# Kernel optimization log

Hardware: AMD Instinct MI355X
Metric: run time of the kernel (lower is better)

## Reference

```python
import jax, jax.numpy as jnp
import numpy as np

N, HID, L, NC = 2048, 256, 4, 10
D0, D1, D2 = HID, HID // 2, HID // 8   # dims for degrees l=0,1,2
H, DH = 4, HID // 4                    # heads for degree-0 attention
F = D0 + D1 + D2                       # invariant feature width
C2 = float(np.sqrt(3.0))


def setup_inputs() -> dict:
    key = jax.random.key(0)
    ks = jax.random.split(key, 16)

    def w(k, shape, fan):
        return jax.random.normal(k, shape, jnp.float32) / np.float32(np.sqrt(fan))

    return {
        "x": jax.random.uniform(ks[0], (N, 118), jnp.float32),
        "pos": jax.random.normal(ks[1], (N, 3), jnp.float32) * 3.0,
        "emb_W": w(ks[2], (118, D0), 118),
        "emb_b": jnp.zeros((D0,), jnp.float32),
        "Wq": w(ks[3], (L, F, H * DH), F),
        "Wk": w(ks[4], (L, F, H * DH), F),
        "Wv0": w(ks[5], (L, D0, D0), D0),
        "Wv1": w(ks[6], (L, D1, D1), D1),
        "Wv2": w(ks[7], (L, D2, D2), D2),
        "Ws1": w(ks[8], (L, D0, D1), D0),
        "Ws2": w(ks[9], (L, D0, D2), D0),
        "Wffa": w(ks[10], (L, D0, 2 * D0), D0),
        "Wffb": w(ks[11], (L, 2 * D0, D0), 2 * D0),
        "Wg": w(ks[12], (L, F, D1 + D2), F),
        "out_W": w(ks[13], (D0, NC), D0),
        "out_b": jnp.zeros((NC,), jnp.float32),
    }


def _sph_harmonics(pos):
    """Real spherical harmonics Y1 [N,N,3], Y2 [N,N,5] of pairwise unit vectors."""
    rel = pos[None, :, :] - pos[:, None, :]                  # [N,N,3]
    dist = jnp.linalg.norm(rel, axis=-1, keepdims=True)
    valid = (dist > 1e-6).astype(pos.dtype)                  # zero out self-pairs
    u = rel / jnp.maximum(dist, 1e-6) * valid
    ux, uy, uz = u[..., 0], u[..., 1], u[..., 2]
    Y1 = u
    Y2 = jnp.stack([
        C2 * ux * uy,
        C2 * uy * uz,
        0.5 * (3.0 * uz * uz - 1.0),
        C2 * ux * uz,
        0.5 * C2 * (ux * ux - uy * uy),
    ], axis=-1) * valid                                      # [N,N,5]
    return Y1, Y2


def _invariants(x0, x1, x2):
    return jnp.concatenate([
        x0,
        jnp.linalg.norm(x1, axis=-1),
        jnp.linalg.norm(x2, axis=-1),
    ], axis=-1)                                              # [N,F]


def _layer(x0, x1, x2, Y1, Y2, Wq, Wk, Wv0, Wv1, Wv2, Ws1, Ws2, Wffa, Wffb, Wg):
    inv = _invariants(x0, x1, x2)
    q = (inv @ Wq).reshape(N, H, DH)
    k = (inv @ Wk).reshape(N, H, DH)
    attn = jax.nn.softmax(jnp.einsum('nhd,mhd->hnm', q, k) / np.float32(np.sqrt(DH)), axis=-1)

    # degree-0 aggregation (4 heads)
    v0 = (x0 @ Wv0).reshape(N, H, D0 // H)
    agg0 = jnp.einsum('hnm,mhc->nhc', attn, v0).reshape(N, D0)

    a = attn.mean(0)                                         # [N,N] single head for l>0
    # degree-1: channel-mixed values + degree-0 -> degree-1 via Y1
    v1 = jnp.einsum('mdc,de->mec', x1, Wv1)                  # [N,D1,3]
    agg1 = jnp.einsum('nm,mdc->ndc', a, v1)
    mix1 = jnp.einsum('nmc,md->ndc', a[:, :, None] * Y1, x0 @ Ws1)
    # degree-2: channel-mixed values + degree-0 -> degree-2 via Y2
    v2 = jnp.einsum('mdc,de->mec', x2, Wv2)                  # [N,D2,5]
    agg2 = jnp.einsum('nm,mdc->ndc', a, v2)
    mix2 = jnp.einsum('nmc,md->ndc', a[:, :, None] * Y2, x0 @ Ws2)

    x0 = x0 + agg0
    x1 = x1 + agg1 + mix1
    x2 = x2 + agg2 + mix2

    # gated equivariant feedforward
    x0 = x0 + jax.nn.silu(x0 @ Wffa) @ Wffb
    g = jax.nn.sigmoid(_invariants(x0, x1, x2) @ Wg)         # [N,D1+D2]
    x1 = x1 * g[:, :D1, None]
    x2 = x2 * g[:, D1:, None]
    return x0, x1, x2


def reference(x, pos, emb_W, emb_b, Wq, Wk, Wv0, Wv1, Wv2, Ws1, Ws2, Wffa, Wffb, Wg, out_W, out_b):
    Y1, Y2 = _sph_harmonics(pos)
    x0 = x @ emb_W + emb_b                                   # input embedding
    x1 = jnp.zeros((N, D1, 3), x0.dtype)
    x2 = jnp.zeros((N, D2, 5), x0.dtype)
    for l in range(L):
        x0, x1, x2 = _layer(x0, x1, x2, Y1, Y2,
                            Wq[l], Wk[l], Wv0[l], Wv1[l], Wv2[l],
                            Ws1[l], Ws2[l], Wffa[l], Wffb[l], Wg[l])
    return x0 @ out_W + out_b                                # [N, num_classes]
```

## Files before the change

### kernel.cpp

```cpp
#include <hip/hip_runtime.h>
#include <math.h>

#define N_    2048
#define D0_   256
#define D1_   128
#define D2_   32
#define F_    416
#define H_    4
#define DH_   64
#define L_    4
#define NC_   10
#define C2_   1.7320508075688772f
#define X12W  544

typedef unsigned short u16;
typedef __attribute__((ext_vector_type(8))) short short8v;
typedef __attribute__((ext_vector_type(4))) float f32x4;

union U8 { u16 u[8]; short8v v; };

__device__ __forceinline__ u16 f2bf(float f) {
    union { float f; unsigned int u; } x; x.f = f;
    unsigned int r = x.u + 0x7FFFu + ((x.u >> 16) & 1u);
    return (u16)(r >> 16);
}
__device__ __forceinline__ float bf2f(u16 u) {
    union { float f; unsigned int u; } x; x.u = ((unsigned int)u) << 16;
    return x.f;
}

__device__ __forceinline__ f32x4 mfma16(short8v a, short8v b, f32x4 c) {
    return __builtin_amdgcn_mfma_f32_16x16x32_bf16(a, b, c, 0, 0, 0);
}

enum { B_NN = 0, B_NT = 1 };
enum { EPI_STORE = 0, EPI_SILU = 1, EPI_SIGMOID = 2, EPI_ACCUM = 3, EPI_ATOMIC = 4,
       EPI_STOREB = 5 };

template<int BLAY, int EPI>
__global__ __launch_bounds__(256) void mfma_gemm(
    const float* __restrict__ A, int lda,
    const float* __restrict__ B, int ldb,
    const float* __restrict__ bias,
    float* __restrict__ C, int ldc,
    int M, int K, int Nn, float scale, int kchunk)
{
    __shared__ __align__(16) u16 As[64][40];
    __shared__ __align__(16) u16 Bs[64][40];
    const int t = threadIdx.x;
    const int bm = blockIdx.y * 64, bn = blockIdx.x * 64;
    const int lane = t & 63, w = t >> 6;
    const int r0 = (w >> 1) * 32, c0 = (w & 1) * 32;
    const int fr = lane & 15, fk = (lane >> 4) * 8;
    const int ml = t >> 2, k8 = (t & 3) * 8;
    const int kbeg = blockIdx.z * kchunk;
    const int kend = (kbeg + kchunk < K) ? kbeg + kchunk : K;
    f32x4 acc[2][2] = {};

    for (int k0 = kbeg; k0 < kend; k0 += 32) {
        {
            U8 u;
            if (((lda & 3) == 0) && (k0 + 32 <= kend)) {
                const float* ap = A + (size_t)(bm + ml) * lda + k0 + k8;
                float4 a0 = *(const float4*)ap;
                float4 a1 = *(const float4*)(ap + 4);
                u.u[0]=f2bf(a0.x); u.u[1]=f2bf(a0.y); u.u[2]=f2bf(a0.z); u.u[3]=f2bf(a0.w);
                u.u[4]=f2bf(a1.x); u.u[5]=f2bf(a1.y); u.u[6]=f2bf(a1.z); u.u[7]=f2bf(a1.w);
            } else {
#pragma unroll
                for (int j = 0; j < 8; ++j) {
                    int kk = k0 + k8 + j;
                    u.u[j] = f2bf(kk < kend ? A[(size_t)(bm + ml) * lda + kk] : 0.f);
                }
            }
            *(short8v*)&As[ml][k8] = u.v;
        }
        {
            U8 u;
            if (BLAY == B_NT) {
                if (((ldb & 3) == 0) && (k0 + 32 <= kend) && (bn + ml < Nn)) {
                    const float* bp = B + (size_t)(bn + ml) * ldb + k0 + k8;
                    float4 b0 = *(const float4*)bp;
                    float4 b1 = *(const float4*)(bp + 4);
                    u.u[0]=f2bf(b0.x); u.u[1]=f2bf(b0.y); u.u[2]=f2bf(b0.z); u.u[3]=f2bf(b0.w);
                    u.u[4]=f2bf(b1.x); u.u[5]=f2bf(b1.y); u.u[6]=f2bf(b1.z); u.u[7]=f2bf(b1.w);
                } else {
#pragma unroll
                    for (int j = 0; j < 8; ++j) {
                        int kk = k0 + k8 + j;
                        u.u[j] = f2bf((kk < kend && bn + ml < Nn)
                                      ? B[(size_t)(bn + ml) * ldb + kk] : 0.f);
                    }
                }
            } else {
                int nc = bn + ml;
#pragma unroll
                for (int j = 0; j < 8; ++j) {
                    int kk = k0 + k8 + j;
                    u.u[j] = f2bf((kk < kend && nc < Nn) ? B[(size_t)kk * ldb + nc] : 0.f);
                }
            }
            *(short8v*)&Bs[ml][k8] = u.v;
        }
        __syncthreads();
        short8v a0 = *(const short8v*)&As[r0 + fr][fk];
        short8v a1 = *(const short8v*)&As[r0 + 16 + fr][fk];
        short8v b0 = *(const short8v*)&Bs[c0 + fr][fk];
        short8v b1 = *(const short8v*)&Bs[c0 + 16 + fr][fk];
        acc[0][0] = mfma16(a0, b0, acc[0][0]);
        acc[0][1] = mfma16(a0, b1, acc[0][1]);
        acc[1][0] = mfma16(a1, b0, acc[1][0]);
        acc[1][1] = mfma16(a1, b1, acc[1][1]);
        __syncthreads();
    }
#pragma unroll
    for (int mi = 0; mi < 2; ++mi)
#pragma unroll
    for (int ni = 0; ni < 2; ++ni)
#pragma unroll
    for (int r = 0; r < 4; ++r) {
        int row = bm + r0 + mi * 16 + ((lane >> 4) << 2) + r;
        int col = bn + c0 + ni * 16 + fr;
        if (col >= Nn) continue;
        float v = acc[mi][ni][r];
        if (EPI == EPI_STOREB) {
            ((u16*)C)[(size_t)row * ldc + col] = f2bf(v * scale);
        } else {
            float* cp = C + (size_t)row * ldc + col;
            if (EPI == EPI_STORE)   *cp = v * scale + (bias ? bias[col] : 0.f);
            if (EPI == EPI_SILU)    *cp = v / (1.f + expf(-v));
            if (EPI == EPI_SIGMOID) *cp = 1.f / (1.f + expf(-v));
            if (EPI == EPI_ACCUM)   *cp += v;
            if (EPI == EPI_ATOMIC)  atomicAdd(cp, v);
        }
    }
}

template<int NB, int EPI>
__global__ __launch_bounds__(256) void aggP(
    const u16* __restrict__ A, int lda,
    const float* __restrict__ B, int ldb,
    float* __restrict__ C, int ldc,
    int K, int Nn, int kchunk)
{
    __shared__ __align__(16) u16 As[64][40];
    __shared__ __align__(16) u16 Bs[NB][64][40];
    const int t = threadIdx.x;
    const int bm = blockIdx.y * 64, bn0 = blockIdx.x * 64 * NB;
    const int lane = t & 63, w = t >> 6;
    const int r0 = (w >> 1) * 32, c0 = (w & 1) * 32;
    const int fr = lane & 15, fk = (lane >> 4) * 8;
    const int ml = t >> 2, k8 = (t & 3) * 8;
    const int kbeg = blockIdx.z * kchunk;
    const int kend = (kbeg + kchunk < K) ? kbeg + kchunk : K;
    f32x4 acc[NB][2][2] = {};

    for (int k0 = kbeg; k0 < kend; k0 += 32) {
        *(short8v*)&As[ml][k8] = *(const short8v*)(A + (size_t)(bm + ml) * lda + k0 + k8);
#pragma unroll
        for (int nb = 0; nb < NB; ++nb) {
            int nc = bn0 + nb * 64 + ml;
            U8 u;
#pragma unroll
            for (int j = 0; j < 8; ++j) {
                int kk = k0 + k8 + j;
                u.u[j] = f2bf(nc < Nn ? B[(size_t)kk * ldb + nc] : 0.f);
            }
            *(short8v*)&Bs[nb][ml][k8] = u.v;
        }
        __syncthreads();
        short8v a0 = *(const short8v*)&As[r0 + fr][fk];
        short8v a1 = *(const short8v*)&As[r0 + 16 + fr][fk];
#pragma unroll
        for (int nb = 0; nb < NB; ++nb) {
            short8v b0 = *(const short8v*)&Bs[nb][c0 + fr][fk];
            short8v b1 = *(const short8v*)&Bs[nb][c0 + 16 + fr][fk];
            acc[nb][0][0] = mfma16(a0, b0, acc[nb][0][0]);
            acc[nb][0][1] = mfma16(a0, b1, acc[nb][0][1]);
            acc[nb][1][0] = mfma16(a1, b0, acc[nb][1][0]);
            acc[nb][1][1] = mfma16(a1, b1, acc[nb][1][1]);
        }
        __syncthreads();
    }
#pragma unroll
    for (int nb = 0; nb < NB; ++nb)
#pragma unroll
    for (int mi = 0; mi < 2; ++mi)
#pragma unroll
    for (int ni = 0; ni < 2; ++ni)
#pragma unroll
    for (int r = 0; r < 4; ++r) {
        int row = bm + r0 + mi * 16 + ((lane >> 4) << 2) + r;
        int col = bn0 + nb * 64 + c0 + ni * 16 + fr;
        if (col >= Nn) continue;
        float v = acc[nb][mi][ni][r];
        float* cp = C + (size_t)row * ldc + col;
        if (EPI == EPI_ATOMIC) atomicAdd(cp, v);
        else                   *cp += v;
    }
}

__global__ void ucompute_kernel(const float* __restrict__ pos, u16* __restrict__ U) {
    int idx = blockIdx.x * 256 + threadIdx.x;
    int n = idx >> 11, m = idx & (N_ - 1);
    float rx = pos[m * 3 + 0] - pos[n * 3 + 0];
    float ry = pos[m * 3 + 1] - pos[n * 3 + 1];
    float rz = pos[m * 3 + 2] - pos[n * 3 + 2];
    float d2 = rx * rx + ry * ry + rz * rz;
    bool valid = d2 > 1e-12f;
    float rinv = valid ? rsqrtf(d2) : 0.f;
    size_t base = (size_t)n * N_ + m;
    const size_t CS = (size_t)N_ * N_;
    U[base]          = f2bf(rx * rinv);
    U[base + CS]     = f2bf(ry * rinv);
    U[base + 2 * CS] = f2bf(rz * rinv);
}

__global__ __launch_bounds__(256) void mix1_kernel(
    const u16* __restrict__ amb, const u16* __restrict__ U,
    const float* __restrict__ s1, float* __restrict__ x12)
{
    const int gx = blockIdx.x;
    const int colbase = (gx & 1) * 64, ks = gx >> 1;
    const int bm = blockIdx.y * 64;
    const size_t CS = (size_t)N_ * N_;
    __shared__ __align__(16) u16 As[3][64][40];
    __shared__ __align__(16) u16 Bs[64][40];
    const int t = threadIdx.x, lane = t & 63, w = t >> 6;
    const int r0 = (w >> 1) * 32, c0 = (w & 1) * 32;
    const int fr = lane & 15, fk = (lane >> 4) * 8;
    const int ml = t >> 2, k8 = (t & 3) * 8;
    const int kbeg = ks * 512, kend = kbeg + 512;
    f32x4 acc[3][2][2] = {};

    for (int m0 = kbeg; m0 < kend; m0 += 32) {
        const size_t off = (size_t)(bm + ml) * N_ + m0 + k8;
        U8 am8; am8.v = *(const short8v*)(amb + off);
        U8 xv, yv, zv;
        xv.v = *(const short8v*)(U + off);
        yv.v = *(const short8v*)(U + CS + off);
        zv.v = *(const short8v*)(U + 2 * CS + off);
        U8 o0, o1, o2;
#pragma unroll
        for (int j = 0; j < 8; ++j) {
            float a = bf2f(am8.u[j]);
            o0.u[j] = f2bf(a * bf2f(xv.u[j]));
            o1.u[j] = f2bf(a * bf2f(yv.u[j]));
            o2.u[j] = f2bf(a * bf2f(zv.u[j]));
        }
        *(short8v*)&As[0][ml][k8] = o0.v;
        *(short8v*)&As[1][ml][k8] = o1.v;
        *(short8v*)&As[2][ml][k8] = o2.v;
        {
            int nc = colbase + ml;
            U8 u;
#pragma unroll
            for (int j = 0; j < 8; ++j)
                u.u[j] = f2bf(s1[(size_t)(m0 + k8 + j) * 128 + nc]);
            *(short8v*)&Bs[ml][k8] = u.v;
        }
        __syncthreads();
        short8v b0 = *(const short8v*)&Bs[c0 + fr][fk];
        short8v b1 = *(const short8v*)&Bs[c0 + 16 + fr][fk];
#pragma unroll
        for (int c = 0; c < 3; ++c) {
            short8v a0 = *(const short8v*)&As[c][r0 + fr][fk];
            short8v a1 = *(const short8v*)&As[c][r0 + 16 + fr][fk];
            acc[c][0][0] = mfma16(a0, b0, acc[c][0][0]);
            acc[c][0][1] = mfma16(a0, b1, acc[c][0][1]);
            acc[c][1][0] = mfma16(a1, b0, acc[c][1][0]);
            acc[c][1][1] = mfma16(a1, b1, acc[c][1][1]);
        }
        __syncthreads();
    }
#pragma unroll
    for (int c = 0; c < 3; ++c)
#pragma unroll
    for (int mi = 0; mi < 2; ++mi)
#pragma unroll
    for (int ni = 0; ni < 2; ++ni)
#pragma unroll
    for (int r = 0; r < 4; ++r) {
        int row = bm + r0 + mi * 16 + ((lane >> 4) << 2) + r;
        int col = colbase + c0 + ni * 16 + fr;
        atomicAdd(&x12[(size_t)row * X12W + col * 3 + c], acc[c][mi][ni][r]);
    }
}

__global__ __launch_bounds__(256) void mix2_kernel(
    const u16* __restrict__ amb, const u16* __restrict__ U,
    const float* __restrict__ s2, float* __restrict__ x12)
{
    const int ks = blockIdx.x;
    const int bm = blockIdx.y * 64;
    const size_t CS = (size_t)N_ * N_;
    __shared__ __align__(16) u16 As[5][64][40];
    __shared__ __align__(16) u16 Bs[64][40];
    const int t = threadIdx.x, lane = t & 63, w = t >> 6;
    const int r0 = (w >> 1) * 32, c0 = (w & 1) * 32;
    const int fr = lane & 15, fk = (lane >> 4) * 8;
    const int ml = t >> 2, k8 = (t & 3) * 8;
    const int kbeg = ks * 256, kend = kbeg + 256;
    f32x4 acc[5][2][2] = {};

    for (int m0 = kbeg; m0 < kend; m0 += 32) {
        const size_t off = (size_t)(bm + ml) * N_ + m0 + k8;
        U8 am8; am8.v = *(const short8v*)(amb + off);
        U8 xv, yv, zv;
        xv.v = *(const short8v*)(U + off);
        yv.v = *(const short8v*)(U + CS + off);
        zv.v = *(const short8v*)(U + 2 * CS + off);
        U8 o[5];
#pragma unroll
        for (int j = 0; j < 8; ++j) {
            float a = bf2f(am8.u[j]);
            float ux = bf2f(xv.u[j]), uy = bf2f(yv.u[j]), uz = bf2f(zv.u[j]);
            o[0].u[j] = f2bf(a * C2_ * ux * uy);
            o[1].u[j] = f2bf(a * C2_ * uy * uz);
            o[2].u[j] = f2bf((ux*ux + uy*uy + uz*uz > 0.5f)
                             ? a * 0.5f * (3.f * uz * uz - 1.f) : 0.f);
            o[3].u[j] = f2bf(a * C2_ * ux * uz);
            o[4].u[j] = f2bf(a * 0.5f * C2_ * (ux * ux - uy * uy));
        }
#pragma unroll
        for (int c = 0; c < 5; ++c) *(short8v*)&As[c][ml][k8] = o[c].v;
        {
            int nc = ml;
            U8 u;
#pragma unroll
            for (int j = 0; j < 8; ++j)
                u.u[j] = f2bf(nc < 32 ? s2[(size_t)(m0 + k8 + j) * 32 + nc] : 0.f);
            *(short8v*)&Bs[ml][k8] = u.v;
        }
        __syncthreads();
        short8v b0 = *(const short8v*)&Bs[c0 + fr][fk];
        short8v b1 = *(const short8v*)&Bs[c0 + 16 + fr][fk];
#pragma unroll
        for (int c = 0; c < 5; ++c) {
            short8v a0 = *(const short8v*)&As[c][r0 + fr][fk];
            short8v a1 = *(const short8v*)&As[c][r0 + 16 + fr][fk];
            acc[c][0][0] = mfma16(a0, b0, acc[c][0][0]);
            acc[c][0][1] = mfma16(a0, b1, acc[c][0][1]);
            acc[c][1][0] = mfma16(a1, b0, acc[c][1][0]);
            acc[c][1][1] = mfma16(a1, b1, acc[c][1][1]);
        }
        __syncthreads();
    }
#pragma unroll
    for (int c = 0; c < 5; ++c)
#pragma unroll
    for (int mi = 0; mi < 2; ++mi)
#pragma unroll
    for (int ni = 0; ni < 2; ++ni)
#pragma unroll
    for (int r = 0; r < 4; ++r) {
        int row = bm + r0 + mi * 16 + ((lane >> 4) << 2) + r;
        int col = c0 + ni * 16 + fr;
        if (col < 32)
            atomicAdd(&x12[(size_t)row * X12W + 384 + col * 5 + c], acc[c][mi][ni][r]);
    }
}

__global__ void invar_kernel(const float* __restrict__ x0, const float* __restrict__ x12,
                             float* __restrict__ inv) {
    int n = blockIdx.x, t = threadIdx.x;
    inv[(size_t)n * F_ + t] = x0[(size_t)n * D0_ + t];
    if (t < 128) {
        const float* p = x12 + (size_t)n * X12W + t * 3;
        inv[(size_t)n * F_ + 256 + t] = sqrtf(p[0]*p[0] + p[1]*p[1] + p[2]*p[2]);
    }
    if (t < 32) {
        const float* p = x12 + (size_t)n * X12W + 384 + t * 5;
        inv[(size_t)n * F_ + 384 + t] =
            sqrtf(p[0]*p[0] + p[1]*p[1] + p[2]*p[2] + p[3]*p[3] + p[4]*p[4]);
    }
}

__global__ void v1_kernel(const float* __restrict__ x12, const float* __restrict__ W,
                          float* __restrict__ Vflat) {
    int m = blockIdx.x, t = threadIdx.x;
    __shared__ float sh[384];
    sh[t] = x12[(size_t)m * X12W + t];
    __syncthreads();
    int e = t / 3, c = t % 3;
    float acc = 0.f;
#pragma unroll 4
    for (int d = 0; d < 128; ++d)
        acc = fmaf(sh[d * 3 + c], W[d * 128 + e], acc);
    Vflat[(size_t)m * X12W + t] = acc;
}

__global__ void v2_kernel(const float* __restrict__ x12, const float* __restrict__ W,
                          float* __restrict__ Vflat) {
    int m = blockIdx.x, t = threadIdx.x;
    __shared__ float sh[160];
    if (t < 160) sh[t] = x12[(size_t)m * X12W + 384 + t];
    __syncthreads();
    if (t < 160) {
        int e = t / 5, c = t % 5;
        float acc = 0.f;
#pragma unroll 4
        for (int d = 0; d < 32; ++d)
            acc = fmaf(sh[d * 5 + c], W[d * 32 + e], acc);
        Vflat[(size_t)m * X12W + 384 + t] = acc;
    }
}

__global__ void softmax4(u16* __restrict__ Sb, u16* __restrict__ amb) {
    int n = blockIdx.x, t = threadIdx.x;
    __shared__ float red[256];
    const size_t NN = (size_t)N_ * N_;
    float amv[8] = {};
    for (int h = 0; h < H_; ++h) {
        u16* Sp = Sb + (size_t)h * NN + (size_t)n * N_ + t * 8;
        U8 sv; sv.v = *(const short8v*)Sp;
        float s[8];
#pragma unroll
        for (int j = 0; j < 8; ++j) s[j] = bf2f(sv.u[j]);
        float mx = s[0];
#pragma unroll
        for (int j = 1; j < 8; ++j) mx = fmaxf(mx, s[j]);
        red[t] = mx; __syncthreads();
        for (int st = 128; st > 0; st >>= 1) { if (t < st) red[t] = fmaxf(red[t], red[t + st]); __syncthreads(); }
        mx = red[0]; __syncthreads();
        float sum = 0.f;
#pragma unroll
        for (int j = 0; j < 8; ++j) { s[j] = expf(s[j] - mx); sum += s[j]; }
        red[t] = sum; __syncthreads();
        for (int st = 128; st > 0; st >>= 1) { if (t < st) red[t] += red[t + st]; __syncthreads(); }
        float rinv = 1.f / red[0]; __syncthreads();
        U8 pv;
#pragma unroll
        for (int j = 0; j < 8; ++j) {
            float p = s[j] * rinv;
            pv.u[j] = f2bf(p);
            amv[j] += 0.25f * p;
        }
        *(short8v*)Sp = pv.v;
    }
    U8 av;
#pragma unroll
    for (int j = 0; j < 8; ++j) av.u[j] = f2bf(amv[j]);
    *(short8v*)(amb + (size_t)n * N_ + t * 8) = av.v;
}

__global__ void gate_kernel(const float* __restrict__ g, float* __restrict__ x12) {
    int idx = blockIdx.x * 256 + threadIdx.x;
    if (idx >= N_ * X12W) return;
    int n = idx / X12W, j = idx % X12W;
    float gv = (j < 384) ? g[n * 160 + j / 3] : g[n * 160 + 128 + (j - 384) / 5];
    x12[idx] *= gv;
}

extern "C" void kernel_launch(void* const* d_in, const int* in_sizes, int n_in,
                              void* d_out, int out_size, void* d_ws, size_t ws_size,
                              hipStream_t stream) {
    const float* x    = (const float*)d_in[0];
    const float* pos  = (const float*)d_in[1];
    const float* embW = (const float*)d_in[2];
    const float* embB = (const float*)d_in[3];
    const float* Wq   = (const float*)d_in[4];
    const float* Wk   = (const float*)d_in[5];
    const float* Wv0  = (const float*)d_in[6];
    const float* Wv1  = (const float*)d_in[7];
    const float* Wv2  = (const float*)d_in[8];
    const float* Ws1  = (const float*)d_in[9];
    const float* Ws2  = (const float*)d_in[10];
    const float* Wffa = (const float*)d_in[11];
    const float* Wffb = (const float*)d_in[12];
    const float* Wg   = (const float*)d_in[13];
    const float* outW = (const float*)d_in[14];
    const float* outB = (const float*)d_in[15];
    float* out = (float*)d_out;

    const size_t NN = (size_t)N_ * N_;
    float* p = (float*)d_ws;
    float* x0    = p; p += N_ * D0_;
    float* x12   = p; p += N_ * X12W;
    float* inv   = p; p += N_ * F_;
    float* q     = p; p += N_ * D0_;
    float* k     = p; p += N_ * D0_;
    float* v0    = p; p += N_ * D0_;
    float* Vflat = p; p += N_ * X12W;
    float* s1    = p; p += N_ * D1_;
    float* s2    = p; p += N_ * D2_;
    float* fft   = p; p += N_ * 512;
    float* gm    = p; p += N_ * 160;
    u16* ub  = (u16*)p;
    u16* Sb  = ub; ub += 4 * NN;
    u16* amb = ub; ub += NN;
    u16* U   = ub;

    hipMemsetAsync(x12, 0, (size_t)N_ * X12W * sizeof(float), stream);
    ucompute_kernel<<<(N_ * N_) / 256, 256, 0, stream>>>(pos, U);

    mfma_gemm<B_NN, EPI_STORE><<<dim3(4, 32), 256, 0, stream>>>(
        x, 118, embW, 256, embB, x0, 256, N_, 118, 256, 1.f, 118);

    for (int l = 0; l < L_; ++l) {
        const float* Wq_l   = Wq   + (size_t)l * F_ * 256;
        const float* Wk_l   = Wk   + (size_t)l * F_ * 256;
        const float* Wv0_l  = Wv0  + (size_t)l * 256 * 256;
        const float* Wv1_l  = Wv1  + (size_t)l * 128 * 128;
        const float* Wv2_l  = Wv2  + (size_t)l * 32 * 32;
        const float* Ws1_l  = Ws1  + (size_t)l * 256 * 128;
        const float* Ws2_l  = Ws2  + (size_t)l * 256 * 32;
        const float* Wffa_l = Wffa + (size_t)l * 256 * 512;
        const float* Wffb_l = Wffb + (size_t)l * 512 * 256;
        const float* Wg_l   = Wg   + (size_t)l * F_ * 160;

        invar_kernel<<<N_, 256, 0, stream>>>(x0, x12, inv);
        mfma_gemm<B_NN, EPI_STORE><<<dim3(4, 32), 256, 0, stream>>>(
            inv, F_, Wq_l, 256, nullptr, q, 256, N_, F_, 256, 1.f, F_);
        mfma_gemm<B_NN, EPI_STORE><<<dim3(4, 32), 256, 0, stream>>>(
            inv, F_, Wk_l, 256, nullptr, k, 256, N_, F_, 256, 1.f, F_);
        mfma_gemm<B_NN, EPI_STORE><<<dim3(4, 32), 256, 0, stream>>>(
            x0, 256, Wv0_l, 256, nullptr, v0, 256, N_, 256, 256, 1.f, 256);
        mfma_gemm<B_NN, EPI_STORE><<<dim3(2, 32), 256, 0, stream>>>(
            x0, 256, Ws1_l, 128, nullptr, s1, 128, N_, 256, 128, 1.f, 256);
        mfma_gemm<B_NN, EPI_STORE><<<dim3(1, 32), 256, 0, stream>>>(
            x0, 256, Ws2_l, 32, nullptr, s2, 32, N_, 256, 32, 1.f, 256);
        v1_kernel<<<N_, 384, 0, stream>>>(x12, Wv1_l, Vflat);
        v2_kernel<<<N_, 192, 0, stream>>>(x12, Wv2_l, Vflat);

        for (int h = 0; h < H_; ++h)
            mfma_gemm<B_NT, EPI_STOREB><<<dim3(32, 32), 256, 0, stream>>>(
                q + h * 64, 256, k + h * 64, 256, nullptr,
                (float*)(Sb + (size_t)h * NN), N_, N_, 64, N_, 0.125f, 64);
        softmax4<<<N_, 256, 0, stream>>>(Sb, amb);
        for (int h = 0; h < H_; ++h)
            aggP<1, EPI_ATOMIC><<<dim3(1, 32, 8), 256, 0, stream>>>(
                Sb + (size_t)h * NN, N_, v0 + h * 64, 256, x0 + h * 64, 256,
                N_, 64, 256);

        aggP<3, EPI_ATOMIC><<<dim3(3, 32, 3), 256, 0, stream>>>(
            amb, N_, Vflat, X12W, x12, X12W, N_, X12W, 704);
        mix1_kernel<<<dim3(8, 32), 256, 0, stream>>>(amb, U, s1, x12);
        mix2_kernel<<<dim3(8, 32), 256, 0, stream>>>(amb, U, s2, x12);

        mfma_gemm<B_NN, EPI_SILU><<<dim3(8, 32), 256, 0, stream>>>(
            x0, 256, Wffa_l, 512, nullptr, fft, 512, N_, 256, 512, 1.f, 256);
        mfma_gemm<B_NN, EPI_ACCUM><<<dim3(4, 32), 256, 0, stream>>>(
            fft, 512, Wffb_l, 256, nullptr, x0, 256, N_, 512, 256, 1.f, 512);

        invar_kernel<<<N_, 256, 0, stream>>>(x0, x12, inv);
        mfma_gemm<B_NN, EPI_SIGMOID><<<dim3(3, 32), 256, 0, stream>>>(
            inv, F_, Wg_l, 160, nullptr, gm, 160, N_, F_, 160, 1.f, F_);
        gate_kernel<<<(N_ * X12W + 255) / 256, 256, 0, stream>>>(gm, x12);
    }

    mfma_gemm<B_NN, EPI_STORE><<<dim3(1, 32), 256, 0, stream>>>(
        x0, 256, outW, NC_, outB, out, NC_, N_, 256, NC_, 1.f, 256);
}
```

Before: 1.766 ms.

## Batch per-head launches via grid z and merge mix kernels into channel-parallel grid

Adds head/k-split decoding of blockIdx.z to the GEMM and aggregation kernels so the four per-head score GEMMs and four aggregation launches become single launches. It merges mix1 and mix2 into one kernel that assigns one spherical-harmonic channel per z-slice, which raises block count but makes each block re-read amb and s1/s2. It also changes the aggP<3> k-split from 3 to 4 chunks. The aim is fewer launches and better occupancy on the GPU, at the cost of redundant global loads per channel.

```diff
diff --git a/kernel.cpp b/kernel.cpp
--- a/kernel.cpp
+++ b/kernel.cpp
@@ -43,17 +43,20 @@
     const float* __restrict__ B, int ldb,
     const float* __restrict__ bias,
     float* __restrict__ C, int ldc,
-    int M, int K, int Nn, float scale, int kchunk)
+    int M, int K, int Nn, float scale, int kchunk,
+    int zk, long long Ah, long long Bh, long long Ch)
 {
     __shared__ __align__(16) u16 As[64][40];
     __shared__ __align__(16) u16 Bs[64][40];
     const int t = threadIdx.x;
     const int bm = blockIdx.y * 64, bn = blockIdx.x * 64;
+    const int hz = blockIdx.z / zk, kz = blockIdx.z % zk;
+    A += (size_t)hz * Ah; B += (size_t)hz * Bh;
     const int lane = t & 63, w = t >> 6;
     const int r0 = (w >> 1) * 32, c0 = (w & 1) * 32;
     const int fr = lane & 15, fk = (lane >> 4) * 8;
     const int ml = t >> 2, k8 = (t & 3) * 8;
-    const int kbeg = blockIdx.z * kchunk;
+    const int kbeg = kz * kchunk;
     const int kend = (kbeg + kchunk < K) ? kbeg + kchunk : K;
     f32x4 acc[2][2] = {};
 
@@ -124,9 +127,9 @@
         if (col >= Nn) continue;
         float v = acc[mi][ni][r];
         if (EPI == EPI_STOREB) {
-            ((u16*)C)[(size_t)row * ldc + col] = f2bf(v * scale);
+            ((u16*)C + (size_t)hz * Ch)[(size_t)row * ldc + col] = f2bf(v * scale);
         } else {
-            float* cp = C + (size_t)row * ldc + col;
+            float* cp = C + (size_t)hz * Ch + (size_t)row * ldc + col;
             if (EPI == EPI_STORE)   *cp = v * scale + (bias ? bias[col] : 0.f);
             if (EPI == EPI_SILU)    *cp = v / (1.f + expf(-v));
             if (EPI == EPI_SIGMOID) *cp = 1.f / (1.f + expf(-v));
@@ -141,17 +144,20 @@
     const u16* __restrict__ A, int lda,
     const float* __restrict__ B, int ldb,
     float* __restrict__ C, int ldc,
-    int K, int Nn, int kchunk)
+    int K, int Nn, int kchunk,
+    int zk, long long Ah, long long Bh, long long Ch)
 {
     __shared__ __align__(16) u16 As[64][40];
     __shared__ __align__(16) u16 Bs[NB][64][40];
     const int t = threadIdx.x;
     const int bm = blockIdx.y * 64, bn0 = blockIdx.x * 64 * NB;
+    const int hz = blockIdx.z / zk, kz = blockIdx.z % zk;
+    A += (size_t)hz * Ah; B += (size_t)hz * Bh; C += (size_t)hz * Ch;
     const int lane = t & 63, w = t >> 6;
     const int r0 = (w >> 1) * 32, c0 = (w & 1) * 32;
     const int fr = lane & 15, fk = (lane >> 4) * 8;
     const int ml = t >> 2, k8 = (t & 3) * 8;
-    const int kbeg = blockIdx.z * kchunk;
+    const int kbeg = kz * kchunk;
     const int kend = (kbeg + kchunk < K) ? kbeg + kchunk : K;
     f32x4 acc[NB][2][2] = {};
 
@@ -216,65 +222,79 @@
     U[base + 2 * CS] = f2bf(rz * rinv);
 }
 
-__global__ __launch_bounds__(256) void mix1_kernel(
+__global__ __launch_bounds__(256) void mixc_kernel(
     const u16* __restrict__ amb, const u16* __restrict__ U,
-    const float* __restrict__ s1, float* __restrict__ x12)
+    const float* __restrict__ s1, const float* __restrict__ s2,
+    float* __restrict__ x12)
 {
+    const int ch = blockIdx.z;
     const int gx = blockIdx.x;
-    const int colbase = (gx & 1) * 64, ks = gx >> 1;
     const int bm = blockIdx.y * 64;
     const size_t CS = (size_t)N_ * N_;
-    __shared__ __align__(16) u16 As[3][64][40];
+    const bool deg1 = ch < 3;
+    const int colbase = deg1 ? (gx & 1) * 64 : 0;
+    const int ks      = deg1 ? (gx >> 1) : gx;
+    const int kchunk  = deg1 ? 512 : 256;
+    const float* Bp   = deg1 ? s1 : s2;
+    const int Bld     = deg1 ? 128 : 32;
+    __shared__ __align__(16) u16 As[64][40];
     __shared__ __align__(16) u16 Bs[64][40];
     const int t = threadIdx.x, lane = t & 63, w = t >> 6;
     const int r0 = (w >> 1) * 32, c0 = (w & 1) * 32;
     const int fr = lane & 15, fk = (lane >> 4) * 8;
     const int ml = t >> 2, k8 = (t & 3) * 8;
-    const int kbeg = ks * 512, kend = kbeg + 512;
-    f32x4 acc[3][2][2] = {};
+    const int kbeg = ks * kchunk, kend = kbeg + kchunk;
+    f32x4 acc[2][2] = {};
 
     for (int m0 = kbeg; m0 < kend; m0 += 32) {
         const size_t off = (size_t)(bm + ml) * N_ + m0 + k8;
         U8 am8; am8.v = *(const short8v*)(amb + off);
-        U8 xv, yv, zv;
-        xv.v = *(const short8v*)(U + off);
-        yv.v = *(const short8v*)(U + CS + off);
-        zv.v = *(const short8v*)(U + 2 * CS + off);
-        U8 o0, o1, o2;
-#pragma unroll
-        for (int j = 0; j < 8; ++j) {
-            float a = bf2f(am8.u[j]);
-            o0.u[j] = f2bf(a * bf2f(xv.u[j]));
-            o1.u[j] = f2bf(a * bf2f(yv.u[j]));
-            o2.u[j] = f2bf(a * bf2f(zv.u[j]));
-        }
-        *(short8v*)&As[0][ml][k8] = o0.v;
-        *(short8v*)&As[1][ml][k8] = o1.v;
-        *(short8v*)&As[2][ml][k8] = o2.v;
+        U8 o;
+        if (deg1) {
+            U8 uv; uv.v = *(const short8v*)(U + (size_t)ch * CS + off);
+#pragma unroll
+            for (int j = 0; j < 8; ++j)
+                o.u[j] = f2bf(bf2f(am8.u[j]) * bf2f(uv.u[j]));
+        } else {
+            U8 xv, yv, zv;
+            xv.v = *(const short8v*)(U + off);
+            yv.v = *(const short8v*)(U + CS + off);
+            zv.v = *(const short8v*)(U + 2 * CS + off);
+#pragma unroll
+            for (int j = 0; j < 8; ++j) {
+                float a = bf2f(am8.u[j]);
+                float ux = bf2f(xv.u[j]), uy = bf2f(yv.u[j]), uz = bf2f(zv.u[j]);
+                float y;
+                if      (ch == 3) y = C2_ * ux * uy;
+                else if (ch == 4) y = C2_ * uy * uz;
+                else if (ch == 5) y = (ux*ux + uy*uy + uz*uz > 0.5f)
+                                      ? 0.5f * (3.f * uz * uz - 1.f) : 0.f;
+                else if (ch == 6) y = C2_ * ux * uz;
+                else              y = 0.5f * C2_ * (ux * ux - uy * uy);
+                o.u[j] = f2bf(a * y);
+            }
+        }
+        *(short8v*)&As[ml][k8] = o.v;
         {
             int nc = colbase + ml;
             U8 u;
 #pragma unroll
             for (int j = 0; j < 8; ++j)
-                u.u[j] = f2bf(s1[(size_t)(m0 + k8 + j) * 128 + nc]);
+                u.u[j] = f2bf((deg1 || nc < 32)
+                              ? Bp[(size_t)(m0 + k8 + j) * Bld + nc] : 0.f);
             *(short8v*)&Bs[ml][k8] = u.v;
         }
         __syncthreads();
+        short8v a0 = *(const short8v*)&As[r0 + fr][fk];
+        short8v a1 = *(const short8v*)&As[r0 + 16 + fr][fk];
         short8v b0 = *(const short8v*)&Bs[c0 + fr][fk];
         short8v b1 = *(const short8v*)&Bs[c0 + 16 + fr][fk];
-#pragma unroll
-        for (int c = 0; c < 3; ++c) {
-            short8v a0 = *(const short8v*)&As[c][r0 + fr][fk];
-            short8v a1 = *(const short8v*)&As[c][r0 + 16 + fr][fk];
-            acc[c][0][0] = mfma16(a0, b0, acc[c][0][0]);
-            acc[c][0][1] = mfma16(a0, b1, acc[c][0][1]);
-            acc[c][1][0] = mfma16(a1, b0, acc[c][1][0]);
-            acc[c][1][1] = mfma16(a1, b1, acc[c][1][1]);
-        }
+        acc[0][0] = mfma16(a0, b0, acc[0][0]);
+        acc[0][1] = mfma16(a0, b1, acc[0][1]);
+        acc[1][0] = mfma16(a1, b0, acc[1][0]);
+        acc[1][1] = mfma16(a1, b1, acc[1][1]);
         __syncthreads();
     }
-#pragma unroll
-    for (int c = 0; c < 3; ++c)
 #pragma unroll
     for (int mi = 0; mi < 2; ++mi)
 #pragma unroll
@@ -283,81 +303,9 @@
     for (int r = 0; r < 4; ++r) {
         int row = bm + r0 + mi * 16 + ((lane >> 4) << 2) + r;
         int col = colbase + c0 + ni * 16 + fr;
-        atomicAdd(&x12[(size_t)row * X12W + col * 3 + c], acc[c][mi][ni][r]);
-    }
-}
-
-__global__ __launch_bounds__(256) void mix2_kernel(
-    const u16* __restrict__ amb, const u16* __restrict__ U,
-    const float* __restrict__ s2, float* __restrict__ x12)
-{
-    const int ks = blockIdx.x;
-    const int bm = blockIdx.y * 64;
-    const size_t CS = (size_t)N_ * N_;
-    __shared__ __align__(16) u16 As[5][64][40];
-    __shared__ __align__(16) u16 Bs[64][40];
-    const int t = threadIdx.x, lane = t & 63, w = t >> 6;
-    const int r0 = (w >> 1) * 32, c0 = (w & 1) * 32;
-    const int fr = lane & 15, fk = (lane >> 4) * 8;
-    const int ml = t >> 2, k8 = (t & 3) * 8;
-    const int kbeg = ks * 256, kend = kbeg + 256;
-    f32x4 acc[5][2][2] = {};
-
-    for (int m0 = kbeg; m0 < kend; m0 += 32) {
-        const size_t off = (size_t)(bm + ml) * N_ + m0 + k8;
-        U8 am8; am8.v = *(const short8v*)(amb + off);
-        U8 xv, yv, zv;
-        xv.v = *(const short8v*)(U + off);
-        yv.v = *(const short8v*)(U + CS + off);
-        zv.v = *(const short8v*)(U + 2 * CS + off);
-        U8 o[5];
-#pragma unroll
-        for (int j = 0; j < 8; ++j) {
-            float a = bf2f(am8.u[j]);
-            float ux = bf2f(xv.u[j]), uy = bf2f(yv.u[j]), uz = bf2f(zv.u[j]);
-            o[0].u[j] = f2bf(a * C2_ * ux * uy);
-            o[1].u[j] = f2bf(a * C2_ * uy * uz);
-            o[2].u[j] = f2bf((ux*ux + uy*uy + uz*uz > 0.5f)
-                             ? a * 0.5f * (3.f * uz * uz - 1.f) : 0.f);
-            o[3].u[j] = f2bf(a * C2_ * ux * uz);
-            o[4].u[j] = f2bf(a * 0.5f * C2_ * (ux * ux - uy * uy));
-        }
-#pragma unroll
-        for (int c = 0; c < 5; ++c) *(short8v*)&As[c][ml][k8] = o[c].v;
-        {
-            int nc = ml;
-            U8 u;
-#pragma unroll
-            for (int j = 0; j < 8; ++j)
-                u.u[j] = f2bf(nc < 32 ? s2[(size_t)(m0 + k8 + j) * 32 + nc] : 0.f);
-            *(short8v*)&Bs[ml][k8] = u.v;
-        }
-        __syncthreads();
-        short8v b0 = *(const short8v*)&Bs[c0 + fr][fk];
-        short8v b1 = *(const short8v*)&Bs[c0 + 16 + fr][fk];
-#pragma unroll
-        for (int c = 0; c < 5; ++c) {
-            short8v a0 = *(const short8v*)&As[c][r0 + fr][fk];
-            short8v a1 = *(const short8v*)&As[c][r0 + 16 + fr][fk];
-            acc[c][0][0] = mfma16(a0, b0, acc[c][0][0]);
-            acc[c][0][1] = mfma16(a0, b1, acc[c][0][1]);
-            acc[c][1][0] = mfma16(a1, b0, acc[c][1][0]);
-            acc[c][1][1] = mfma16(a1, b1, acc[c][1][1]);
-        }
-        __syncthreads();
-    }
-#pragma unroll
-    for (int c = 0; c < 5; ++c)
-#pragma unroll
-    for (int mi = 0; mi < 2; ++mi)
-#pragma unroll
-    for (int ni = 0; ni < 2; ++ni)
-#pragma unroll
-    for (int r = 0; r < 4; ++r) {
-        int row = bm + r0 + mi * 16 + ((lane >> 4) << 2) + r;
-        int col = c0 + ni * 16 + fr;
-        if (col < 32)
-            atomicAdd(&x12[(size_t)row * X12W + 384 + col * 5 + c], acc[c][mi][ni][r]);
+        float v = acc[mi][ni][r];
+        if (deg1)          atomicAdd(&x12[(size_t)row * X12W + col * 3 + ch], v);
+        else if (col < 32) atomicAdd(&x12[(size_t)row * X12W + 384 + col * 5 + (ch - 3)], v);
     }
 }
 
@@ -495,7 +443,7 @@
     ucompute_kernel<<<(N_ * N_) / 256, 256, 0, stream>>>(pos, U);
 
     mfma_gemm<B_NN, EPI_STORE><<<dim3(4, 32), 256, 0, stream>>>(
-        x, 118, embW, 256, embB, x0, 256, N_, 118, 256, 1.f, 118);
+        x, 118, embW, 256, embB, x0, 256, N_, 118, 256, 1.f, 118, 1, 0, 0, 0);
 
     for (int l = 0; l < L_; ++l) {
         const float* Wq_l   = Wq   + (size_t)l * F_ * 256;
@@ -511,44 +459,42 @@
 
         invar_kernel<<<N_, 256, 0, stream>>>(x0, x12, inv);
         mfma_gemm<B_NN, EPI_STORE><<<dim3(4, 32), 256, 0, stream>>>(
-            inv, F_, Wq_l, 256, nullptr, q, 256, N_, F_, 256, 1.f, F_);
+            inv, F_, Wq_l, 256, nullptr, q, 256, N_, F_, 256, 1.f, F_, 1, 0, 0, 0);
         mfma_gemm<B_NN, EPI_STORE><<<dim3(4, 32), 256, 0, stream>>>(
-            inv, F_, Wk_l, 256, nullptr, k, 256, N_, F_, 256, 1.f, F_);
+            inv, F_, Wk_l, 256, nullptr, k, 256, N_, F_, 256, 1.f, F_, 1, 0, 0, 0);
         mfma_gemm<B_NN, EPI_STORE><<<dim3(4, 32), 256, 0, stream>>>(
-            x0, 256, Wv0_l, 256, nullptr, v0, 256, N_, 256, 256, 1.f, 256);
+            x0, 256, Wv0_l, 256, nullptr, v0, 256, N_, 256, 256, 1.f, 256, 1, 0, 0, 0);
         mfma_gemm<B_NN, EPI_STORE><<<dim3(2, 32), 256, 0, stream>>>(
-            x0, 256, Ws1_l, 128, nullptr, s1, 128, N_, 256, 128, 1.f, 256);
+            x0, 256, Ws1_l, 128, nullptr, s1, 128, N_, 256, 128, 1.f, 256, 1, 0, 0, 0);
         mfma_gemm<B_NN, EPI_STORE><<<dim3(1, 32), 256, 0, stream>>>(
-            x0, 256, Ws2_l, 32, nullptr, s2, 32, N_, 256, 32, 1.f, 256);
+            x0, 256, Ws2_l, 32, nullptr, s2, 32, N_, 256, 32, 1.f, 256, 1, 0, 0, 0);
         v1_kernel<<<N_, 384, 0, stream>>>(x12, Wv1_l, Vflat);
         v2_kernel<<<N_, 192, 0, stream>>>(x12, Wv2_l, Vflat);
 
-        for (int h = 0; h < H_; ++h)
-            mfma_gemm<B_NT, EPI_STOREB><<<dim3(32, 32), 256, 0, stream>>>(
-                q + h * 64, 256, k + h * 64, 256, nullptr,
-                (float*)(Sb + (size_t)h * NN), N_, N_, 64, N_, 0.125f, 64);
+        mfma_gemm<B_NT, EPI_STOREB><<<dim3(32, 32, 4), 256, 0, stream>>>(
+            q, 256, k, 256, nullptr, (float*)Sb, N_, N_, 64, N_, 0.125f, 64,
+            1, 64, 64, (long long)NN);
         softmax4<<<N_, 256, 0, stream>>>(Sb, amb);
-        for (int h = 0; h < H_; ++h)
-            aggP<1, EPI_ATOMIC><<<dim3(1, 32, 8), 256, 0, stream>>>(
-                Sb + (size_t)h * NN, N_, v0 + h * 64, 256, x0 + h * 64, 256,
-                N_, 64, 256);
-
-        aggP<3, EPI_ATOMIC><<<dim3(3, 32, 3), 256, 0, stream>>>(
-            amb, N_, Vflat, X12W, x12, X12W, N_, X12W, 704);
-        mix1_kernel<<<dim3(8, 32), 256, 0, stream>>>(amb, U, s1, x12);
-        mix2_kernel<<<dim3(8, 32), 256, 0, stream>>>(amb, U, s2, x12);
+        aggP<1, EPI_ATOMIC><<<dim3(1, 32, 32), 256, 0, stream>>>(
+            Sb, N_, v0, 256, x0, 256, N_, 64, 256,
+            8, (long long)NN, 64, 64);
+
+        aggP<3, EPI_ATOMIC><<<dim3(3, 32, 4), 256, 0, stream>>>(
+            amb, N_, Vflat, X12W, x12, X12W, N_, X12W, 512,
+            4, 0, 0, 0);
+        mixc_kernel<<<dim3(8, 32, 8), 256, 0, stream>>>(amb, U, s1, s2, x12);
 
         mfma_gemm<B_NN, EPI_SILU><<<dim3(8, 32), 256, 0, stream>>>(
-            x0, 256, Wffa_l, 512, nullptr, fft, 512, N_, 256, 512, 1.f, 256);
+            x0, 256, Wffa_l, 512, nullptr, fft, 512, N_, 256, 512, 1.f, 256, 1, 0, 0, 0);
         mfma_gemm<B_NN, EPI_ACCUM><<<dim3(4, 32), 256, 0, stream>>>(
-            fft, 512, Wffb_l, 256, nullptr, x0, 256, N_, 512, 256, 1.f, 512);
+            fft, 512, Wffb_l, 256, nullptr, x0, 256, N_, 512, 256, 1.f, 512, 1, 0, 0, 0);
 
         invar_kernel<<<N_, 256, 0, stream>>>(x0, x12, inv);
         mfma_gemm<B_NN, EPI_SIGMOID><<<dim3(3, 32), 256, 0, stream>>>(
-            inv, F_, Wg_l, 160, nullptr, gm, 160, N_, F_, 160, 1.f, F_);
+            inv, F_, Wg_l, 160, nullptr, gm, 160, N_, F_, 160, 1.f, F_, 1, 0, 0, 0);
         gate_kernel<<<(N_ * X12W + 255) / 256, 256, 0, stream>>>(gm, x12);
     }
 
     mfma_gemm<B_NN, EPI_STORE><<<dim3(1, 32), 256, 0, stream>>>(
-        x0, 256, outW, NC_, outB, out, NC_, N_, 256, NC_, 1.f, 256);
-}
+        x0, 256, outW, NC_, outB, out, NC_, N_, 256, NC_, 1.f, 256, 1, 0, 0, 0);
+}
```

After: 1.569 ms. -11.2%, faster.
